# Kernel optimization log

Hardware: AMD Instinct MI355X
Metric: run time of the kernel (lower is better)

## Reference

```python
import jax, jax.numpy as jnp
import numpy as np

B, T, C = 4, 2048, 768
H, D = 6, 128


def apply_rotary_emb(x, cos, sin):
    # x: (B, T, H, D); cos, sin: (1, T, 1, D//2)
    d = x.shape[-1] // 2
    x1, x2 = x[..., :d], x[..., d:]
    y1 = x1 * cos + x2 * sin
    y2 = -x1 * sin + x2 * cos
    return jnp.concatenate([y1, y2], axis=-1)


def rmsnorm(x):
    eps = 1e-15
    ms = jnp.mean(x * x, axis=-1, keepdims=True)
    return x / jnp.sqrt(ms + eps)


def setup_inputs() -> dict:
    key = jax.random.key(0)
    ks = jax.random.split(key, 7)
    s = 0.02
    return {
        "x": jax.random.normal(ks[0], (B, T, C), jnp.float32),
        "cos": jax.random.normal(ks[1], (1, T, 1, D // 2), jnp.float32),
        "sin": jax.random.normal(ks[2], (1, T, 1, D // 2), jnp.float32),
        "Wq": jax.random.normal(ks[3], (C, C), jnp.float32) * s,
        "Wk": jax.random.normal(ks[4], (C, C), jnp.float32) * s,
        "Wv": jax.random.normal(ks[5], (C, C), jnp.float32) * s,
        "Wo": jax.random.normal(ks[6], (C, C), jnp.float32) * s,
    }


def reference(x, cos, sin, Wq, Wk, Wv, Wo):
    b, t, c = x.shape
    # QKV projections (nn.Linear: x @ W.T)
    q = (x @ Wq.T).reshape(b, t, H, D)
    k = (x @ Wk.T).reshape(b, t, H, D)
    v = (x @ Wv.T).reshape(b, t, H, D)
    # RoPE then QK-RMSNorm
    q = rmsnorm(apply_rotary_emb(q, cos, sin))
    k = rmsnorm(apply_rotary_emb(k, cos, sin))
    # (B, H, T, D)
    q = q.transpose(0, 2, 1, 3)
    k = k.transpose(0, 2, 1, 3)
    v = v.transpose(0, 2, 1, 3)
    scores = jnp.einsum('bhqd,bhkd->bhqk', q, k) / jnp.sqrt(jnp.float32(D))
    causal = jnp.tril(jnp.ones((t, t), dtype=bool))
    scores = jnp.where(causal[None, None], scores, -jnp.inf)
    attn = jax.nn.softmax(scores, axis=-1)
    out = jnp.einsum('bhqk,bhkd->bhqd', attn, v)
    out = out.transpose(0, 2, 1, 3).reshape(b, t, c)
    return out @ Wo.T
```

## Files before the change

### kernel.cpp

```cpp
#include <hip/hip_runtime.h>

#define T_SEQ 2048
#define NH    6
#define HD    128
#define CDIM  768
#define NQKV  2304
#define MROWS 8192
#define NSLOT 1104

typedef __attribute__((ext_vector_type(8)))  short bf16x8;
typedef __attribute__((ext_vector_type(4)))  float f32x4;
typedef __attribute__((ext_vector_type(16))) float f32x16;
typedef __attribute__((ext_vector_type(2)))  int   i32x2;

__device__ __forceinline__ unsigned short f2bf(float f){
  unsigned int u = __builtin_bit_cast(unsigned int, f);
  u += 0x7fffu + ((u >> 16) & 1u);
  return (unsigned short)(u >> 16);
}
__device__ __forceinline__ float bf2f(unsigned short h){
  unsigned int u = ((unsigned int)h) << 16;
  return __builtin_bit_cast(float, u);
}
__device__ __forceinline__ unsigned int cvtpk(float lo, float hi){
  unsigned int r;
  asm("v_cvt_pk_bf16_f32 %0, %1, %2" : "=v"(r) : "v"(lo), "v"(hi));
  return r;
}

__device__ __forceinline__ void gload_lds16(const void* g, void* l){
  __builtin_amdgcn_global_load_lds(
      (const __attribute__((address_space(1))) unsigned int*)g,
      (__attribute__((address_space(3))) unsigned int*)l, 16, 0, 0);
}

__device__ __forceinline__ int ncq(int Q){
  return Q < 3 ? 1 : Q < 7 ? 2 : Q < 10 ? 3 : Q < 14 ? 4 : 5;
}
__device__ __forceinline__ int cumc(int Q){
  return Q < 4 ? Q : Q < 8 ? 3 + 2*(Q-3) : Q < 11 ? 11 + 3*(Q-7)
       : Q < 15 ? 20 + 4*(Q-10) : 36 + 5*(Q-14);
}

__global__ __launch_bounds__(256) void cvt_f32_bf16(
    const float* __restrict__ in, unsigned short* __restrict__ out, int n4){
  int i = blockIdx.x * 256 + threadIdx.x;
  if (i >= n4) return;
  float4 v = reinterpret_cast<const float4*>(in)[i];
  ushort4 o;
  o.x = f2bf(v.x); o.y = f2bf(v.y); o.z = f2bf(v.z); o.w = f2bf(v.w);
  reinterpret_cast<ushort4*>(out)[i] = o;
}

__global__ __launch_bounds__(256) void cvt_w4(
    const float* __restrict__ w0, const float* __restrict__ w1,
    const float* __restrict__ w2, const float* __restrict__ w3,
    unsigned short* __restrict__ out){
  const int which = blockIdx.y;
  const float* src = which == 0 ? w0 : which == 1 ? w1 : which == 2 ? w2 : w3;
  int i = blockIdx.x * 256 + threadIdx.x;
  float4 v = reinterpret_cast<const float4*>(src)[i];
  ushort4 o;
  o.x = f2bf(v.x); o.y = f2bf(v.y); o.z = f2bf(v.z); o.w = f2bf(v.w);
  reinterpret_cast<ushort4*>(out + (size_t)which * CDIM * CDIM)[i] = o;
}

template<int BF16OUT>
__global__ __launch_bounds__(256) void gemm_bt(
    const unsigned short* __restrict__ A,
    const unsigned short* __restrict__ B,
    void* __restrict__ Cv, int M, int N, int K)
{
  __shared__ unsigned short As[128 * 64];
  __shared__ unsigned short Bs[128 * 64];
  const int tid  = threadIdx.x;
  const int lane = tid & 63;
  const int wave = tid >> 6;
  const int wm = wave >> 1, wn = wave & 1;
  const int lr = lane & 15, lg = lane >> 4;
  const int srow = lane >> 3;
  const int sslot = (lane & 7) ^ (lane >> 3);
  const int gx = gridDim.x, gy = gridDim.y, nwg = gx * gy;
  const int flat = blockIdx.y * gx + blockIdx.x;
  const int nf = (flat & 7) * (nwg >> 3) + (flat >> 3);
  const int row0 = (nf / gy) * 128, col0 = (nf % gy) * 128;

  f32x4 acc[4][4];
  const f32x4 z = {0.f, 0.f, 0.f, 0.f};
  #pragma unroll
  for (int i = 0; i < 4; ++i)
    #pragma unroll
    for (int j = 0; j < 4; ++j) acc[i][j] = z;

  for (int k0 = 0; k0 < K; k0 += 64){
    #pragma unroll
    for (int i = 0; i < 4; ++i){
      int seg = wave * 4 + i;
      int r = seg * 8 + srow;
      gload_lds16(&A[(size_t)(row0 + r) * K + k0 + sslot * 8], &As[seg * 512]);
      gload_lds16(&B[(size_t)(col0 + r) * K + k0 + sslot * 8], &Bs[seg * 512]);
    }
    __syncthreads();
    #pragma unroll
    for (int kk = 0; kk < 64; kk += 32){
      bf16x8 af[4], bfr[4];
      #pragma unroll
      for (int mi = 0; mi < 4; ++mi)
        af[mi] = *reinterpret_cast<const bf16x8*>(
            &As[(wm*64 + mi*16 + lr) * 64 + ((((kk>>3) + lg) ^ (lr & 7)) * 8)]);
      #pragma unroll
      for (int ni = 0; ni < 4; ++ni)
        bfr[ni] = *reinterpret_cast<const bf16x8*>(
            &Bs[(wn*64 + ni*16 + lr) * 64 + ((((kk>>3) + lg) ^ (lr & 7)) * 8)]);
      #pragma unroll
      for (int mi = 0; mi < 4; ++mi)
        #pragma unroll
        for (int ni = 0; ni < 4; ++ni)
          acc[mi][ni] = __builtin_amdgcn_mfma_f32_16x16x32_bf16(af[mi], bfr[ni], acc[mi][ni], 0, 0, 0);
    }
    __syncthreads();
  }
  #pragma unroll
  for (int mi = 0; mi < 4; ++mi){
    #pragma unroll
    for (int ni = 0; ni < 4; ++ni){
      #pragma unroll
      for (int r = 0; r < 4; ++r){
        int row = row0 + wm*64 + mi*16 + lg*4 + r;
        int col = col0 + wn*64 + ni*16 + lr;
        if (BF16OUT)
          reinterpret_cast<unsigned short*>(Cv)[(size_t)row * N + col] = f2bf(acc[mi][ni][r]);
        else
          reinterpret_cast<float*>(Cv)[(size_t)row * N + col] = acc[mi][ni][r];
      }
    }
  }
}

__global__ __launch_bounds__(256) void rope_rms(
    unsigned short* __restrict__ QKVb,
    const float* __restrict__ cosp, const float* __restrict__ sinp)
{
  const int bt    = blockIdx.x;
  const int task  = blockIdx.y * 4 + (threadIdx.x >> 6);
  const int which = task / NH;
  const int h     = task % NH;
  const int t     = bt & (T_SEQ - 1);
  const int lane  = threadIdx.x & 63;
  unsigned short* p = QKVb + (size_t)bt * NQKV + which * CDIM + h * HD;
  float x1 = bf2f(p[lane]);
  float x2 = bf2f(p[lane + 64]);
  float c = cosp[t * 64 + lane];
  float s = sinp[t * 64 + lane];
  float y1 = x1 * c + x2 * s;
  float y2 = x2 * c - x1 * s;
  float ss = y1 * y1 + y2 * y2;
  #pragma unroll
  for (int off = 1; off < 64; off <<= 1) ss += __shfl_xor(ss, off);
  float inv = rsqrtf(ss * (1.0f / 128.0f) + 1e-15f);
  p[lane]      = f2bf(y1 * inv);
  p[lane + 64] = f2bf(y2 * inv);
}

__global__ __launch_bounds__(256) void transpose_v(
    const unsigned short* __restrict__ QKVb, unsigned short* __restrict__ Vt)
{
  __shared__ unsigned short tile[64][66];
  const int tid = threadIdx.x;
  const int t0  = blockIdx.x * 64;
  const int hd  = blockIdx.y;
  const int b   = blockIdx.z;
  const int h = hd >> 1, dhalf = (hd & 1) * 64;
  const unsigned short* src = QKVb + (size_t)b * T_SEQ * NQKV + 2 * CDIM + h * HD + dhalf;
  #pragma unroll
  for (int it = 0; it < 2; ++it){
    int ch = tid + it * 256;
    int r = ch >> 3, cc = (ch & 7) * 8;
    *reinterpret_cast<int4*>(&tile[r][cc]) =
        *reinterpret_cast<const int4*>(&src[(size_t)(t0 + r) * NQKV + cc]);
  }
  __syncthreads();
  unsigned short* dst = Vt + ((size_t)(b * NH + h) * HD + dhalf) * T_SEQ + t0;
  #pragma unroll
  for (int it = 0; it < 2; ++it){
    int ch = tid + it * 256;
    int d = ch >> 3, cc = (ch & 7) * 8;
    union { int4 v; unsigned short u[8]; } w;
    #pragma unroll
    for (int j = 0; j < 8; ++j) w.u[j] = tile[cc + j][d];
    *reinterpret_cast<int4*>(&dst[(size_t)d * T_SEQ + cc]) = w.v;
  }
}

__global__ __launch_bounds__(256) void attn_fwd(
    const unsigned short* __restrict__ QKVb,
    const unsigned short* __restrict__ Vt,
    unsigned short* __restrict__ AO,
    unsigned short* __restrict__ Op, float* __restrict__ Mp, float* __restrict__ Lp)
{
  __shared__ unsigned short Ks[64][136];
  __shared__ unsigned short Vs[128][72];
  const int tid = threadIdx.x;
  const int lane = tid & 63, wave = tid >> 6;
  const int l31 = lane & 31, hi = lane >> 5;

  const int flat = blockIdx.x;
  const int nf = (flat & 7) * 138 + (flat >> 3);
  const int bh = nf / 46;
  const int L = 45 - (nf % 46);
  int Q, c;
  if (L < 3)      { Q = L; c = 0; }
  else if (L < 11){ int m = L - 3;  Q = 3 + (m >> 1);  c = m & 1; }
  else if (L < 20){ int m = L - 11; Q = 7 + m / 3;     c = m % 3; }
  else if (L < 36){ int m = L - 20; Q = 10 + (m >> 2); c = m & 3; }
  else            { int m = L - 36; Q = 14 + m / 5;    c = m % 5; }
  const int nc = ncq(Q);
  const int tiles = 2 * Q + 2;
  const int base = tiles / nc, rem = tiles % nc;
  const int tbeg = c * base + (c < rem ? c : rem);
  const int tend = tbeg + base + (c < rem ? 1 : 0);
  const int b = bh / NH, h = bh % NH;
  const int qw = Q * 128 + wave * 32;

  const unsigned short* Qp = QKVb + (size_t)(b * T_SEQ) * NQKV + h * HD;
  const unsigned short* Kp = QKVb + (size_t)(b * T_SEQ) * NQKV + CDIM + h * HD;
  const unsigned short* Vp = Vt + (size_t)bh * HD * T_SEQ;

  bf16x8 qf[8];
  #pragma unroll
  for (int c4 = 0; c4 < 8; ++c4)
    qf[c4] = *reinterpret_cast<const bf16x8*>(
        &Qp[(size_t)(qw + l31) * NQKV + c4 * 16 + hi * 8]);

  f32x16 o[4];
  #pragma unroll
  for (int db = 0; db < 4; ++db)
    #pragma unroll
    for (int r = 0; r < 16; ++r) o[db][r] = 0.f;
  float mrun = -__builtin_inff(), lrun = 0.f;
  const float scl = 0.08838834764831845f;

  for (int t = tbeg; t < tend; ++t){
    const int kv0 = t * 64;
    #pragma unroll
    for (int it = 0; it < 4; ++it){
      int ch = tid + it * 256;
      int r = ch >> 4, cc = (ch & 15) * 8;
      *reinterpret_cast<int4*>(&Ks[r][cc]) =
          *reinterpret_cast<const int4*>(&Kp[(size_t)(kv0 + r) * NQKV + cc]);
      int rv = ch >> 3, cv = (ch & 7) * 8;
      *reinterpret_cast<int4*>(&Vs[rv][cv]) =
          *reinterpret_cast<const int4*>(&Vp[(size_t)rv * T_SEQ + kv0 + cv]);
    }
    __syncthreads();

    if (kv0 <= qw + 31){
      f32x16 s[2];
      #pragma unroll
      for (int r = 0; r < 16; ++r){ s[0][r] = 0.f; s[1][r] = 0.f; }
      __builtin_amdgcn_s_setprio(1);
      #pragma unroll
      for (int c4 = 0; c4 < 8; ++c4){
        bf16x8 k0 = *reinterpret_cast<const bf16x8*>(&Ks[l31][c4 * 16 + hi * 8]);
        bf16x8 k1 = *reinterpret_cast<const bf16x8*>(&Ks[32 + l31][c4 * 16 + hi * 8]);
        s[0] = __builtin_amdgcn_mfma_f32_32x32x16_bf16(k0, qf[c4], s[0], 0, 0, 0);
        s[1] = __builtin_amdgcn_mfma_f32_32x32x16_bf16(k1, qf[c4], s[1], 0, 0, 0);
      }
      __builtin_amdgcn_s_setprio(0);

      const int qg = qw + l31;
      if (kv0 + 63 > qw){
        #pragma unroll
        for (int blk = 0; blk < 2; ++blk)
          #pragma unroll
          for (int r = 0; r < 16; ++r){
            int kg = kv0 + 32 * blk + (r & 3) + 8 * (r >> 2) + 4 * hi;
            s[blk][r] = (kg <= qg) ? s[blk][r] * scl : -__builtin_inff();
          }
      } else {
        #pragma unroll
        for (int blk = 0; blk < 2; ++blk)
          #pragma unroll
          for (int r = 0; r < 16; ++r) s[blk][r] *= scl;
      }

      float t8[8];
      #pragma unroll
      for (int blk = 0; blk < 2; ++blk)
        #pragma unroll
        for (int j = 0; j < 4; ++j)
          t8[blk * 4 + j] = fmaxf(fmaxf(s[blk][4*j], s[blk][4*j+1]),
                                  fmaxf(s[blk][4*j+2], s[blk][4*j+3]));
      float pm = fmaxf(fmaxf(fmaxf(t8[0], t8[1]), fmaxf(t8[2], t8[3])),
                       fmaxf(fmaxf(t8[4], t8[5]), fmaxf(t8[6], t8[7])));
      pm = fmaxf(pm, __shfl_xor(pm, 32));

      if (__any(pm > mrun)){
        float mn = fmaxf(mrun, pm);
        float scf = (mrun == -__builtin_inff()) ? 0.f : __expf(mrun - mn);
        mrun = mn; lrun *= scf;
        #pragma unroll
        for (int r = 0; r < 16; ++r){
          float scr = __shfl(scf, (r & 3) + 8 * (r >> 2) + 4 * hi, 32);
          #pragma unroll
          for (int db = 0; db < 4; ++db) o[db][r] *= scr;
        }
      }

      float a8[8];
      #pragma unroll
      for (int blk = 0; blk < 2; ++blk)
        #pragma unroll
        for (int j = 0; j < 4; ++j){
          float p0 = __expf(s[blk][4*j]   - mrun);
          float p1 = __expf(s[blk][4*j+1] - mrun);
          float p2 = __expf(s[blk][4*j+2] - mrun);
          float p3 = __expf(s[blk][4*j+3] - mrun);
          s[blk][4*j] = p0; s[blk][4*j+1] = p1; s[blk][4*j+2] = p2; s[blk][4*j+3] = p3;
          a8[blk * 4 + j] = (p0 + p1) + (p2 + p3);
        }
      float ls = ((a8[0] + a8[1]) + (a8[2] + a8[3])) + ((a8[4] + a8[5]) + (a8[6] + a8[7]));
      lrun += ls + __shfl_xor(ls, 32);

      __builtin_amdgcn_s_setprio(1);
      #pragma unroll
      for (int kc = 0; kc < 4; ++kc){
        const int blk = kc >> 1, base2 = (kc & 1) * 8;
        unsigned int a0 = cvtpk(s[blk][base2+0], s[blk][base2+1]);
        unsigned int b0 = cvtpk(s[blk][base2+4], s[blk][base2+5]);
        unsigned int a1 = cvtpk(s[blk][base2+2], s[blk][base2+3]);
        unsigned int b1 = cvtpk(s[blk][base2+6], s[blk][base2+7]);
        i32x2 sw0 = __builtin_amdgcn_permlane32_swap((int)a0, (int)b0, false, false);
        i32x2 sw1 = __builtin_amdgcn_permlane32_swap((int)a1, (int)b1, false, false);
        union { bf16x8 v; unsigned int u[4]; } pa;
        pa.u[0] = (unsigned int)sw0[0];
        pa.u[1] = (unsigned int)sw1[0];
        pa.u[2] = (unsigned int)sw0[1];
        pa.u[3] = (unsigned int)sw1[1];
        #pragma unroll
        for (int db = 0; db < 4; ++db){
          bf16x8 vf = *reinterpret_cast<const bf16x8*>(
              &Vs[db * 32 + l31][kc * 16 + hi * 8]);
          o[db] = __builtin_amdgcn_mfma_f32_32x32x16_bf16(pa.v, vf, o[db], 0, 0, 0);
        }
      }
      __builtin_amdgcn_s_setprio(0);
    }
    __syncthreads();
  }

  if (nc == 1){
    float inv = 1.0f / lrun;
    #pragma unroll
    for (int r = 0; r < 16; ++r){
      const int crow = (r & 3) + 8 * (r >> 2) + 4 * hi;
      float ir = __shfl(inv, crow, 32);
      #pragma unroll
      for (int db = 0; db < 4; ++db)
        AO[((size_t)b * T_SEQ + qw + crow) * CDIM + h * HD + db * 32 + l31] =
            f2bf(o[db][r] * ir);
    }
  } else {
    const int slot = bh * 46 + cumc(Q) + c;
    unsigned short* OpW = Op + (size_t)slot * 128 * 128;
    #pragma unroll
    for (int r = 0; r < 16; ++r){
      const int row = wave * 32 + (r & 3) + 8 * (r >> 2) + 4 * hi;
      #pragma unroll
      for (int db = 0; db < 4; ++db)
        OpW[row * 128 + db * 32 + l31] = f2bf(o[db][r]);
    }
    if (hi == 0){
      Mp[(size_t)slot * 128 + wave * 32 + l31] = mrun;
      Lp[(size_t)slot * 128 + wave * 32 + l31] = lrun;
    }
  }
}

__global__ __launch_bounds__(256) void attn_combine(
    const unsigned short* __restrict__ Op, const float* __restrict__ Mp,
    const float* __restrict__ Lp, unsigned short* __restrict__ AO)
{
  const int Q  = 3 + blockIdx.x;
  const int bh = blockIdx.y;
  const int b = bh / NH, h = bh % NH;
  const int nc = ncq(Q);
  const int slot0 = bh * 46 + cumc(Q);
  #pragma unroll
  for (int u = 0; u < 16; ++u){
    int unit = threadIdx.x + u * 256;
    int r = unit >> 5, d4 = unit & 31;
    float m = -__builtin_inff();
    for (int cc = 0; cc < nc; ++cc)
      m = fmaxf(m, Mp[(size_t)(slot0 + cc) * 128 + r]);
    float l = 0.f;
    float a0 = 0.f, a1 = 0.f, a2 = 0.f, a3 = 0.f;
    for (int cc = 0; cc < nc; ++cc){
      float w = __expf(Mp[(size_t)(slot0 + cc) * 128 + r] - m);
      l += w * Lp[(size_t)(slot0 + cc) * 128 + r];
      const ushort4 v = *reinterpret_cast<const ushort4*>(
          &Op[((size_t)(slot0 + cc) * 128 + r) * 128 + d4 * 4]);
      a0 += w * bf2f(v.x); a1 += w * bf2f(v.y);
      a2 += w * bf2f(v.z); a3 += w * bf2f(v.w);
    }
    float inv = 1.0f / l;
    ushort4 ov;
    ov.x = f2bf(a0 * inv); ov.y = f2bf(a1 * inv);
    ov.z = f2bf(a2 * inv); ov.w = f2bf(a3 * inv);
    *reinterpret_cast<ushort4*>(
        &AO[((size_t)b * T_SEQ + Q * 128 + r) * CDIM + h * HD + d4 * 4]) = ov;
  }
}

extern "C" void kernel_launch(void* const* d_in, const int* in_sizes, int n_in,
                              void* d_out, int out_size, void* d_ws, size_t ws_size,
                              hipStream_t stream)
{
  (void)in_sizes; (void)n_in; (void)out_size; (void)ws_size;
  const float* x    = (const float*)d_in[0];
  const float* cosp = (const float*)d_in[1];
  const float* sinp = (const float*)d_in[2];
  const float* Wq   = (const float*)d_in[3];
  const float* Wk   = (const float*)d_in[4];
  const float* Wv   = (const float*)d_in[5];
  const float* Wo   = (const float*)d_in[6];
  float* out = (float*)d_out;

  unsigned short* xb    = (unsigned short*)d_ws;
  unsigned short* Wqkvb = xb    + (size_t)MROWS * CDIM;
  unsigned short* Wob   = Wqkvb + (size_t)NQKV * CDIM;
  unsigned short* QKVb  = Wob   + (size_t)CDIM * CDIM;
  unsigned short* Vtb   = QKVb  + (size_t)MROWS * NQKV;
  unsigned short* AO    = Vtb   + (size_t)MROWS * CDIM;
  unsigned short* Op    = AO    + (size_t)MROWS * CDIM;
  float* Mp = (float*)(Op + (size_t)NSLOT * 128 * 128);
  float* Lp = Mp + (size_t)NSLOT * 128;

  int n4x = MROWS * CDIM / 4;
  cvt_f32_bf16<<<(n4x + 255) / 256, 256, 0, stream>>>(x, xb, n4x);
  cvt_w4<<<dim3(CDIM * CDIM / 4 / 256, 4), 256, 0, stream>>>(Wq, Wk, Wv, Wo, Wqkvb);

  gemm_bt<1><<<dim3(MROWS / 128, NQKV / 128), 256, 0, stream>>>(xb, Wqkvb, QKVb, MROWS, NQKV, CDIM);
  rope_rms<<<dim3(MROWS, 3), 256, 0, stream>>>(QKVb, cosp, sinp);
  transpose_v<<<dim3(T_SEQ / 64, 12, 4), 256, 0, stream>>>(QKVb, Vtb);
  attn_fwd<<<NSLOT, 256, 0, stream>>>(QKVb, Vtb, AO, Op, Mp, Lp);
  attn_combine<<<dim3(13, 24), 256, 0, stream>>>(Op, Mp, Lp, AO);
  gemm_bt<0><<<dim3(MROWS / 128, CDIM / 128), 256, 0, stream>>>(AO, Wob, out, MROWS, CDIM, CDIM);
}
```

Before: 221.0 us.

## Fuse RoPE and QK-RMSNorm into QKV GEMM epilogue

Removes the separate rope_rms kernel and applies rotary embedding plus RMS normalization in the QKV GEMM epilogue for Q and K column tiles. To do this, the GEMM wave layout changes from a 2x2 split to four waves each owning 32 rows by all 128 columns, so each wave holds a full head row. This saves a launch and a full read-modify-write pass over Q/K in bf16, and normalizes from fp32 accumulators before rounding. In exchange, the B-fragment LDS reads per wave double and the epilogue loads cos/sin per row, which may slow the GEMM itself.

```diff
diff --git a/kernel.cpp b/kernel.cpp
--- a/kernel.cpp
+++ b/kernel.cpp
@@ -65,18 +65,18 @@
   reinterpret_cast<ushort4*>(out + (size_t)which * CDIM * CDIM)[i] = o;
 }
 
-template<int BF16OUT>
+template<int EPI>
 __global__ __launch_bounds__(256) void gemm_bt(
     const unsigned short* __restrict__ A,
     const unsigned short* __restrict__ B,
-    void* __restrict__ Cv, int M, int N, int K)
+    void* __restrict__ Cv, int M, int N, int K,
+    const float* __restrict__ cosp, const float* __restrict__ sinp)
 {
   __shared__ unsigned short As[128 * 64];
   __shared__ unsigned short Bs[128 * 64];
   const int tid  = threadIdx.x;
   const int lane = tid & 63;
   const int wave = tid >> 6;
-  const int wm = wave >> 1, wn = wave & 1;
   const int lr = lane & 15, lg = lane >> 4;
   const int srow = lane >> 3;
   const int sslot = (lane & 7) ^ (lane >> 3);
@@ -84,13 +84,14 @@
   const int flat = blockIdx.y * gx + blockIdx.x;
   const int nf = (flat & 7) * (nwg >> 3) + (flat >> 3);
   const int row0 = (nf / gy) * 128, col0 = (nf % gy) * 128;
-
-  f32x4 acc[4][4];
+  const int wrow = wave * 32;
+
+  f32x4 acc[2][8];
   const f32x4 z = {0.f, 0.f, 0.f, 0.f};
   #pragma unroll
-  for (int i = 0; i < 4; ++i)
-    #pragma unroll
-    for (int j = 0; j < 4; ++j) acc[i][j] = z;
+  for (int i = 0; i < 2; ++i)
+    #pragma unroll
+    for (int j = 0; j < 8; ++j) acc[i][j] = z;
 
   for (int k0 = 0; k0 < K; k0 += 64){
     #pragma unroll
@@ -103,63 +104,76 @@
     __syncthreads();
     #pragma unroll
     for (int kk = 0; kk < 64; kk += 32){
-      bf16x8 af[4], bfr[4];
-      #pragma unroll
-      for (int mi = 0; mi < 4; ++mi)
+      bf16x8 af[2], bfr[8];
+      #pragma unroll
+      for (int mi = 0; mi < 2; ++mi)
         af[mi] = *reinterpret_cast<const bf16x8*>(
-            &As[(wm*64 + mi*16 + lr) * 64 + ((((kk>>3) + lg) ^ (lr & 7)) * 8)]);
-      #pragma unroll
-      for (int ni = 0; ni < 4; ++ni)
+            &As[(wrow + mi*16 + lr) * 64 + ((((kk>>3) + lg) ^ (lr & 7)) * 8)]);
+      #pragma unroll
+      for (int ni = 0; ni < 8; ++ni)
         bfr[ni] = *reinterpret_cast<const bf16x8*>(
-            &Bs[(wn*64 + ni*16 + lr) * 64 + ((((kk>>3) + lg) ^ (lr & 7)) * 8)]);
-      #pragma unroll
-      for (int mi = 0; mi < 4; ++mi)
-        #pragma unroll
-        for (int ni = 0; ni < 4; ++ni)
+            &Bs[(ni*16 + lr) * 64 + ((((kk>>3) + lg) ^ (lr & 7)) * 8)]);
+      #pragma unroll
+      for (int mi = 0; mi < 2; ++mi)
+        #pragma unroll
+        for (int ni = 0; ni < 8; ++ni)
           acc[mi][ni] = __builtin_amdgcn_mfma_f32_16x16x32_bf16(af[mi], bfr[ni], acc[mi][ni], 0, 0, 0);
     }
     __syncthreads();
   }
-  #pragma unroll
-  for (int mi = 0; mi < 4; ++mi){
-    #pragma unroll
-    for (int ni = 0; ni < 4; ++ni){
-      #pragma unroll
-      for (int r = 0; r < 4; ++r){
-        int row = row0 + wm*64 + mi*16 + lg*4 + r;
-        int col = col0 + wn*64 + ni*16 + lr;
-        if (BF16OUT)
-          reinterpret_cast<unsigned short*>(Cv)[(size_t)row * N + col] = f2bf(acc[mi][ni][r]);
-        else
-          reinterpret_cast<float*>(Cv)[(size_t)row * N + col] = acc[mi][ni][r];
+
+  if (EPI == 0){
+    float* Cf = reinterpret_cast<float*>(Cv);
+    #pragma unroll
+    for (int mi = 0; mi < 2; ++mi)
+      #pragma unroll
+      for (int ni = 0; ni < 8; ++ni)
+        #pragma unroll
+        for (int r = 0; r < 4; ++r)
+          Cf[(size_t)(row0 + wrow + mi*16 + lg*4 + r) * N + col0 + ni*16 + lr] = acc[mi][ni][r];
+  } else {
+    unsigned short* Cb = reinterpret_cast<unsigned short*>(Cv);
+    const int ct = col0 >> 7;
+    if (ct >= 12){
+      #pragma unroll
+      for (int mi = 0; mi < 2; ++mi)
+        #pragma unroll
+        for (int ni = 0; ni < 8; ++ni)
+          #pragma unroll
+          for (int r = 0; r < 4; ++r)
+            Cb[(size_t)(row0 + wrow + mi*16 + lg*4 + r) * N + col0 + ni*16 + lr] =
+                f2bf(acc[mi][ni][r]);
+    } else {
+      #pragma unroll
+      for (int mi = 0; mi < 2; ++mi){
+        #pragma unroll
+        for (int r = 0; r < 4; ++r){
+          const int row = row0 + wrow + mi*16 + lg*4 + r;
+          const int t = row & (T_SEQ - 1);
+          float y1[4], y2[4], ssp = 0.f;
+          #pragma unroll
+          for (int ni = 0; ni < 4; ++ni){
+            const int d = ni*16 + lr;
+            float c = cosp[t * 64 + d];
+            float s = sinp[t * 64 + d];
+            float x1 = acc[mi][ni][r], x2 = acc[mi][ni+4][r];
+            y1[ni] = x1 * c + x2 * s;
+            y2[ni] = x2 * c - x1 * s;
+            ssp += y1[ni]*y1[ni] + y2[ni]*y2[ni];
+          }
+          #pragma unroll
+          for (int off = 1; off < 16; off <<= 1) ssp += __shfl_xor(ssp, off);
+          const float inv = rsqrtf(ssp * (1.0f / 128.0f) + 1e-15f);
+          #pragma unroll
+          for (int ni = 0; ni < 4; ++ni){
+            const int d = ni*16 + lr;
+            Cb[(size_t)row * N + col0 + d]      = f2bf(y1[ni] * inv);
+            Cb[(size_t)row * N + col0 + d + 64] = f2bf(y2[ni] * inv);
+          }
+        }
       }
     }
   }
-}
-
-__global__ __launch_bounds__(256) void rope_rms(
-    unsigned short* __restrict__ QKVb,
-    const float* __restrict__ cosp, const float* __restrict__ sinp)
-{
-  const int bt    = blockIdx.x;
-  const int task  = blockIdx.y * 4 + (threadIdx.x >> 6);
-  const int which = task / NH;
-  const int h     = task % NH;
-  const int t     = bt & (T_SEQ - 1);
-  const int lane  = threadIdx.x & 63;
-  unsigned short* p = QKVb + (size_t)bt * NQKV + which * CDIM + h * HD;
-  float x1 = bf2f(p[lane]);
-  float x2 = bf2f(p[lane + 64]);
-  float c = cosp[t * 64 + lane];
-  float s = sinp[t * 64 + lane];
-  float y1 = x1 * c + x2 * s;
-  float y2 = x2 * c - x1 * s;
-  float ss = y1 * y1 + y2 * y2;
-  #pragma unroll
-  for (int off = 1; off < 64; off <<= 1) ss += __shfl_xor(ss, off);
-  float inv = rsqrtf(ss * (1.0f / 128.0f) + 1e-15f);
-  p[lane]      = f2bf(y1 * inv);
-  p[lane + 64] = f2bf(y2 * inv);
 }
 
 __global__ __launch_bounds__(256) void transpose_v(
@@ -440,10 +454,11 @@
   cvt_f32_bf16<<<(n4x + 255) / 256, 256, 0, stream>>>(x, xb, n4x);
   cvt_w4<<<dim3(CDIM * CDIM / 4 / 256, 4), 256, 0, stream>>>(Wq, Wk, Wv, Wo, Wqkvb);
 
-  gemm_bt<1><<<dim3(MROWS / 128, NQKV / 128), 256, 0, stream>>>(xb, Wqkvb, QKVb, MROWS, NQKV, CDIM);
-  rope_rms<<<dim3(MROWS, 3), 256, 0, stream>>>(QKVb, cosp, sinp);
+  gemm_bt<1><<<dim3(MROWS / 128, NQKV / 128), 256, 0, stream>>>(
+      xb, Wqkvb, QKVb, MROWS, NQKV, CDIM, cosp, sinp);
   transpose_v<<<dim3(T_SEQ / 64, 12, 4), 256, 0, stream>>>(QKVb, Vtb);
   attn_fwd<<<NSLOT, 256, 0, stream>>>(QKVb, Vtb, AO, Op, Mp, Lp);
   attn_combine<<<dim3(13, 24), 256, 0, stream>>>(Op, Mp, Lp, AO);
-  gemm_bt<0><<<dim3(MROWS / 128, CDIM / 128), 256, 0, stream>>>(AO, Wob, out, MROWS, CDIM, CDIM);
-}
+  gemm_bt<0><<<dim3(MROWS / 128, CDIM / 128), 256, 0, stream>>>(
+      AO, Wob, out, MROWS, CDIM, CDIM, nullptr, nullptr);
+}
```

Result: faster. 214.5 us (-2.9%).
